# Optimization experiments

Hardware: AMD Instinct MI355X
Metric: run time of the kernel (lower is better)

## Reference

```python
import jax, jax.numpy as jnp
import numpy as np

B, C, D, Hh, W = 2, 320, 4, 16, 16
N = D * Hh * W          # 1024 nodes
NH = 8                  # num_heads
DH = C // NH            # 40
L = 2                   # num_layers
A, EPD = 16, 64         # da_prior tokens, encode_prior_dim
EDGE_SCALE = 32 ** -0.5 # GraphEdgeFeature dim_head=32
SCALE = DH ** -0.5
EPS = 1e-5


def _ln(x, g, b):
    m = x.mean(-1, keepdims=True)
    v = ((x - m) ** 2).mean(-1, keepdims=True)
    return (x - m) * jax.lax.rsqrt(v + EPS) * g + b


def setup_inputs() -> dict:
    key = jax.random.key(0)
    ks = jax.random.split(key, 16)
    std = 0.02 / np.sqrt(L)
    inp = {
        'x': jax.random.normal(ks[0], (B, C, D, Hh, W), jnp.float32),
        'da_prior': jax.random.normal(ks[1], (B, A, EPD), jnp.float32),
        # GraphEdgeFeature.to_qk (no bias), init std 0.02/sqrt(24)
        'qk_w': jax.random.normal(ks[2], (2 * C, C), jnp.float32) * (0.02 / np.sqrt(24)),
        # fc_prior
        'fcp_w': jax.random.normal(ks[3], (C, EPD), jnp.float32) * 0.02,
        'fcp_b': jnp.zeros((C,), jnp.float32),
        # per-layer (stacked over L)
        'ln1_g': jnp.ones((L, C), jnp.float32),
        'ln1_b': jnp.zeros((L, C), jnp.float32),
        'gln_g': jnp.ones((L, C), jnp.float32),
        'gln_b': jnp.zeros((L, C), jnp.float32),
        'qkv_w': jax.random.normal(ks[4], (L, 3 * C, C), jnp.float32) * std,
        'qkv_b': jnp.zeros((L, 3 * C), jnp.float32),
        'proj_w': jax.random.normal(ks[5], (L, C, C), jnp.float32) * std,
        'proj_b': jnp.zeros((L, C), jnp.float32),
        # expand Conv2d(1, NH, 1): weight [NH], bias [NH]
        'exp_w': jax.random.normal(ks[6], (L, NH), jnp.float32),
        'exp_b': jnp.zeros((L, NH), jnp.float32),
        # reduce Conv2d(NH, 1, 1): weight [NH], bias scalar
        'red_w': jax.random.normal(ks[7], (L, NH), jnp.float32) / np.sqrt(NH),
        'red_b': jnp.zeros((L,), jnp.float32),
    }
    return inp


def _forward(x, da_prior, qk_w, fcp_w, fcp_b, ln1_g, ln1_b, gln_g, gln_b,
             qkv_w, qkv_b, proj_w, proj_b, exp_w, exp_b, red_w, red_b):
    node = x.reshape(B, C, N)                       # [B,C,N]
    # ---- GraphEdgeFeature: full-dim QK attention over nodes ----
    xt = node.transpose(0, 2, 1)                    # [B,N,C]
    qk = xt @ qk_w.T                                # [B,N,2C]
    q_e, k_e = jnp.split(qk, 2, axis=-1)
    edge = jax.nn.softmax(jnp.einsum('bqc,bkc->bqk', q_e, k_e) * EDGE_SCALE, axis=-1)  # [B,N,N]
    # ---- fc_prior ----
    da = da_prior @ fcp_w.T + fcp_b                 # [B,A,C]
    s = da.sum(axis=1)                              # [B,C] (sum over 'a' in einsum bnc,bca->bnc)
    for l in range(L):
        # block norm1 over channel dim
        nt = _ln(node.transpose(0, 2, 1), ln1_g[l], ln1_b[l])   # [B,N,C]
        # torch.einsum('bnn,bnc->bnc') takes the DIAGONAL of edge
        diag = jnp.diagonal(edge, axis1=1, axis2=2)             # [B,N]
        node2 = diag[:, :, None] * nt * s[:, None, :] + nt      # [B,N,C]
        y = _ln(node2, gln_g[l], gln_b[l])
        qkv = (y @ qkv_w[l].T + qkv_b[l]).reshape(B, N, 3, NH, DH)
        qkv = qkv.transpose(2, 0, 3, 1, 4)                      # [3,B,H,N,DH]
        q, k, v = qkv[0], qkv[1], qkv[2]
        attn = jnp.einsum('bhnd,bhmd->bhnm', q, k) * SCALE
        attn = attn + edge[:, None] * exp_w[l][None, :, None, None] + exp_b[l][None, :, None, None]
        a = jax.nn.softmax(attn, axis=-1)                       # [B,H,N,N]
        node_out = jnp.einsum('bhnm,bhmd->bhnd', a, v).transpose(0, 2, 1, 3).reshape(B, N, C)
        edge_new = jnp.einsum('bhnm,h->bnm', a + attn, red_w[l]) + red_b[l]  # [B,N,N]
        ws = jax.nn.softmax(edge_new, axis=-1)
        wsum = (ws * edge_new).sum(-1)                          # [B,N]
        node_out = node_out + wsum[:, :, None]                  # fc=Identity, broadcast
        node_out = node_out @ proj_w[l].T + proj_b[l]
        node = node_out.transpose(0, 2, 1)                      # [B,C,N]
        edge = edge + edge_new
    return node.reshape(B, C, D, Hh, W)


def reference(x, da_prior, qk_w, fcp_w, fcp_b, ln1_g, ln1_b, gln_g, gln_b,
              qkv_w, qkv_b, proj_w, proj_b, exp_w, exp_b, red_w, red_b):
    return _forward(x, da_prior, qk_w, fcp_w, fcp_b, ln1_g, ln1_b, gln_g, gln_b,
                    qkv_w, qkv_b, proj_w, proj_b, exp_w, exp_b, red_w, red_b)
```

## Files before the change

### kernel.cpp

```cpp
#include <hip/hip_runtime.h>
#include <math.h>

#define EDGE_SCALE 0.17677669529663687f
#define ATT_SCALE  0.15811388300841897f
#define LN_EPS 1e-5f

typedef __attribute__((ext_vector_type(8))) short bf8;
typedef __attribute__((ext_vector_type(4))) float f32x4;

__device__ __forceinline__ f32x4 mfma16(bf8 a, bf8 b, f32x4 c) {
  return __builtin_amdgcn_mfma_f32_16x16x32_bf16(a, b, c, 0, 0, 0);
}
__device__ __forceinline__ unsigned short f2bf(float f) {
  union { float f; unsigned u; } v; v.f = f;
  unsigned r = v.u + 0x7FFF + ((v.u >> 16) & 1);
  return (unsigned short)(r >> 16);
}
__device__ __forceinline__ float bf2f(unsigned short h) {
  union { unsigned u; float f; } v; v.u = ((unsigned)h) << 16;
  return v.f;
}
__device__ __forceinline__ float wave_max(float v) {
  #pragma unroll
  for (int o = 32; o > 0; o >>= 1) v = fmaxf(v, __shfl_xor(v, o));
  return v;
}
__device__ __forceinline__ float wave_sum(float v) {
  #pragma unroll
  for (int o = 32; o > 0; o >>= 1) v += __shfl_xor(v, o);
  return v;
}

__global__ __launch_bounds__(256) void k_trans(const float* __restrict__ x,
    float* __restrict__ node, unsigned short* __restrict__ nodebf) {
  __shared__ float tile[32][33];
  const int b = blockIdx.z;
  const int n0 = blockIdx.x * 32, c0 = blockIdx.y * 32;
  const int tx = threadIdx.x & 31, ty = threadIdx.x >> 5;
  #pragma unroll
  for (int k = 0; k < 4; ++k) {
    int c = c0 + ty + 8 * k;
    tile[ty + 8 * k][tx] = x[((size_t)b * 320 + c) * 1024 + n0 + tx];
  }
  __syncthreads();
  #pragma unroll
  for (int k = 0; k < 4; ++k) {
    int n = n0 + ty + 8 * k;
    float v = tile[tx][ty + 8 * k];
    size_t idx = ((size_t)b * 1024 + n) * 320 + c0 + tx;
    node[idx] = v;
    nodebf[idx] = f2bf(v);
  }
}

__global__ __launch_bounds__(320) void k_svec(const float* __restrict__ da,
    const float* __restrict__ fw, const float* __restrict__ fb, float* __restrict__ sv) {
  __shared__ float ds[64];
  const int b = blockIdx.x, t = threadIdx.x;
  if (t < 64) {
    float a = 0.f;
    #pragma unroll
    for (int i = 0; i < 16; ++i) a += da[b * 1024 + i * 64 + t];
    ds[t] = a;
  }
  __syncthreads();
  if (t < 320) {
    float acc = 16.f * fb[t];
    #pragma unroll
    for (int e = 0; e < 64; ++e) acc = fmaf(ds[e], fw[t * 64 + e], acc);
    sv[b * 320 + t] = acc;
  }
}

__global__ void k_wcvt(const float* __restrict__ a, int na,
                       const float* __restrict__ b, int nb,
                       const float* __restrict__ c, int nc,
                       unsigned short* __restrict__ out) {
  int tot = na + nb + nc;
  for (int i = blockIdx.x * blockDim.x + threadIdx.x; i < tot; i += gridDim.x * blockDim.x) {
    float v = (i < na) ? a[i] : ((i < na + nb) ? b[i - na] : c[i - na - nb]);
    out[i] = f2bf(v);
  }
}

__global__ __launch_bounds__(256, 4) void k_mgemm(
    const unsigned short* __restrict__ A, const unsigned short* __restrict__ W,
    const float* __restrict__ bias, void* p0, void* p1, void* p2, int mode) {
  __shared__ float smem[64 * 65];
  const int t = threadIdx.x, w = t >> 6, lane = t & 63;
  const int q16 = lane >> 4, l16 = lane & 15;
  const int rt = blockIdx.x * 64, jt = blockIdx.y * 64;
  f32x4 acc[4];
  #pragma unroll
  for (int i = 0; i < 4; ++i)
    #pragma unroll
    for (int j = 0; j < 4; ++j) acc[i][j] = 0.f;
  const unsigned short* ap = A + (size_t)(rt + 16 * w + l16) * 320 + q16 * 8;
  const unsigned short* wp = W + (size_t)(jt + l16) * 320 + q16 * 8;
  for (int kc = 0; kc < 10; ++kc) {
    bf8 af = *(const bf8*)(ap + kc * 32);
    #pragma unroll
    for (int ct = 0; ct < 4; ++ct) {
      bf8 bf = *(const bf8*)(wp + (size_t)ct * 16 * 320 + kc * 32);
      acc[ct] = mfma16(af, bf, acc[ct]);
    }
  }
  if (mode == 0 || mode == 1) {
    #pragma unroll
    for (int ct = 0; ct < 4; ++ct) {
      int col = jt + ct * 16 + l16;
      float bv = bias ? bias[col] : 0.f;
      #pragma unroll
      for (int r = 0; r < 4; ++r) {
        int row = rt + 16 * w + q16 * 4 + r;
        float v = acc[ct][r] + bv;
        if (mode == 0) {
          ((float*)p0)[(size_t)row * 320 + col] = v;
        } else {
          if (col < 320) ((unsigned short*)p0)[(size_t)row * 320 + col] = f2bf(v);
          else           ((unsigned short*)p1)[(size_t)row * 320 + col - 320] = f2bf(v);
        }
      }
    }
  } else if (mode == 2) {
    const int part = jt / 320;
    if (part < 2) {
      unsigned short* dst = (unsigned short*)(part == 0 ? p0 : p1);
      #pragma unroll
      for (int ct = 0; ct < 4; ++ct) {
        int col = jt + ct * 16 + l16;
        float bv = bias[col];
        int rem = col - part * 320;
        int h = rem / 40, d = rem % 40;
        #pragma unroll
        for (int r = 0; r < 4; ++r) {
          int row = rt + 16 * w + q16 * 4 + r;
          int b = row >> 10, n = row & 1023;
          size_t base = (((size_t)b * 8 + h) * 1024 + n) * 64;
          dst[base + d] = f2bf(acc[ct][r] + bv);
          if (d < 24) dst[base + 40 + d] = 0;
        }
      }
    } else {
      unsigned short* vt_t = (unsigned short*)smem;
      #pragma unroll
      for (int ct = 0; ct < 4; ++ct) {
        int col = jt + ct * 16 + l16;
        float bv = bias[col];
        #pragma unroll
        for (int r = 0; r < 4; ++r)
          vt_t[(ct * 16 + l16) * 72 + 16 * w + q16 * 4 + r] = f2bf(acc[ct][r] + bv);
      }
      __syncthreads();
      const int cl = t >> 2, seg = t & 3;
      int rem = (jt - 640) + cl;
      int h = rem / 40, d = rem % 40;
      int b = rt >> 10, n = (rt & 1023) + seg * 16;
      const float4* lp = (const float4*)&vt_t[cl * 72 + seg * 16];
      float4 a0 = lp[0], a1 = lp[1];
      float4* gp = (float4*)((unsigned short*)p2 +
                             (((size_t)b * 8 + h) * 48 + d) * 1024 + n);
      gp[0] = a0; gp[1] = a1;
    }
  } else {
    #pragma unroll
    for (int ct = 0; ct < 4; ++ct) {
      int col = jt + ct * 16 + l16;
      float bv = bias[col];
      #pragma unroll
      for (int r = 0; r < 4; ++r)
        smem[(16 * w + q16 * 4 + r) * 65 + ct * 16 + l16] = acc[ct][r] + bv;
    }
    __syncthreads();
    const int cl = t >> 2, seg = t & 3;
    int b = rt >> 10, n = (rt & 1023) + seg * 16;
    float* orow = (float*)p0 + ((size_t)b * 320 + jt + cl) * 1024 + n;
    #pragma unroll
    for (int i2 = 0; i2 < 4; ++i2) {
      float4 vv;
      vv.x = smem[(seg * 16 + i2 * 4 + 0) * 65 + cl];
      vv.y = smem[(seg * 16 + i2 * 4 + 1) * 65 + cl];
      vv.z = smem[(seg * 16 + i2 * 4 + 2) * 65 + cl];
      vv.w = smem[(seg * 16 + i2 * 4 + 3) * 65 + cl];
      ((float4*)orow)[i2] = vv;
    }
  }
}

__global__ __launch_bounds__(256, 4) void k_sgemm(
    const unsigned short* __restrict__ qe, const unsigned short* __restrict__ ke,
    float* __restrict__ S) {
  const int t = threadIdx.x, w = t >> 6, lane = t & 63;
  const int q16 = lane >> 4, l16 = lane & 15;
  const int rt = blockIdx.x * 64, jt = blockIdx.y * 64, b = blockIdx.z;
  const unsigned short* A = qe + (size_t)b * 1024 * 320;
  const unsigned short* W = ke + (size_t)b * 1024 * 320;
  f32x4 acc[4];
  #pragma unroll
  for (int i = 0; i < 4; ++i)
    #pragma unroll
    for (int j = 0; j < 4; ++j) acc[i][j] = 0.f;
  const unsigned short* ap = A + (size_t)(rt + 16 * w + l16) * 320 + q16 * 8;
  const unsigned short* wp = W + (size_t)(jt + l16) * 320 + q16 * 8;
  for (int kc = 0; kc < 10; ++kc) {
    bf8 af = *(const bf8*)(ap + kc * 32);
    #pragma unroll
    for (int ct = 0; ct < 4; ++ct) {
      bf8 bf = *(const bf8*)(wp + (size_t)ct * 16 * 320 + kc * 32);
      acc[ct] = mfma16(af, bf, acc[ct]);
    }
  }
  #pragma unroll
  for (int ct = 0; ct < 4; ++ct)
    #pragma unroll
    for (int r = 0; r < 4; ++r)
      S[((size_t)b * 1024 + rt + 16 * w + q16 * 4 + r) * 1024 + jt + ct * 16 + l16] =
          acc[ct][r] * EDGE_SCALE;
}

__global__ __launch_bounds__(256) void k_smax(const float* __restrict__ S,
                                              float* __restrict__ edge) {
  const int w = threadIdx.x >> 6, lane = threadIdx.x & 63;
  const int row = blockIdx.x * 4 + w;
  const float4* sp = (const float4*)(S + (size_t)row * 1024) + lane;
  float4 v[4];
  #pragma unroll
  for (int i = 0; i < 4; ++i) v[i] = sp[i * 64];
  float mx = -3.4e38f;
  #pragma unroll
  for (int i = 0; i < 4; ++i)
    mx = fmaxf(mx, fmaxf(fmaxf(v[i].x, v[i].y), fmaxf(v[i].z, v[i].w)));
  mx = wave_max(mx);
  float s = 0.f;
  #pragma unroll
  for (int i = 0; i < 4; ++i) {
    v[i].x = __expf(v[i].x - mx); v[i].y = __expf(v[i].y - mx);
    v[i].z = __expf(v[i].z - mx); v[i].w = __expf(v[i].w - mx);
    s += v[i].x + v[i].y + v[i].z + v[i].w;
  }
  s = wave_sum(s);
  float inv = 1.f / s;
  float4* ep = (float4*)(edge + (size_t)row * 1024) + lane;
  #pragma unroll
  for (int i = 0; i < 4; ++i)
    ep[i * 64] = make_float4(v[i].x * inv, v[i].y * inv, v[i].z * inv, v[i].w * inv);
}

__global__ __launch_bounds__(256) void k_ln(const float* __restrict__ node,
    const float* __restrict__ edge, const float* __restrict__ sv,
    const float* __restrict__ g1, const float* __restrict__ b1,
    const float* __restrict__ g2, const float* __restrict__ b2,
    unsigned short* __restrict__ y) {
  const int w = threadIdx.x >> 6, lane = threadIdx.x & 63;
  const int row = blockIdx.x * 4 + w;
  const int b = row >> 10, n = row & 1023;
  const float* xr = node + (size_t)row * 320;
  float x[5];
  #pragma unroll
  for (int i = 0; i < 5; ++i) x[i] = xr[lane + 64 * i];
  float s = x[0] + x[1] + x[2] + x[3] + x[4];
  float mean = wave_sum(s) * (1.f / 320.f);
  float v = 0.f;
  #pragma unroll
  for (int i = 0; i < 5; ++i) { float d = x[i] - mean; v += d * d; }
  float rstd = rsqrtf(wave_sum(v) * (1.f / 320.f) + LN_EPS);
  float diag = edge[(size_t)row * 1024 + n];
  float n2[5];
  #pragma unroll
  for (int i = 0; i < 5; ++i) {
    int c = lane + 64 * i;
    float nt = (x[i] - mean) * rstd * g1[c] + b1[c];
    n2[i] = diag * nt * sv[b * 320 + c] + nt;
  }
  s = n2[0] + n2[1] + n2[2] + n2[3] + n2[4];
  float mean2 = wave_sum(s) * (1.f / 320.f);
  v = 0.f;
  #pragma unroll
  for (int i = 0; i < 5; ++i) { float d = n2[i] - mean2; v += d * d; }
  float rstd2 = rsqrtf(wave_sum(v) * (1.f / 320.f) + LN_EPS);
  unsigned short* yr = y + (size_t)row * 320;
  #pragma unroll
  for (int i = 0; i < 5; ++i) {
    int c = lane + 64 * i;
    yr[c] = f2bf((n2[i] - mean2) * rstd2 * g2[c] + b2[c]);
  }
}

__global__ __launch_bounds__(256, 4) void k_score(
    const unsigned short* __restrict__ qbf, const unsigned short* __restrict__ kbf,
    const unsigned short* __restrict__ vtb, const float* __restrict__ edge,
    unsigned short* __restrict__ thbuf, float* __restrict__ att,
    const float* __restrict__ ew, const float* __restrict__ eb,
    const float* __restrict__ rw) {
  __shared__ unsigned short a_lds[4][4][16][20];
  __shared__ unsigned short th_lds[4][16][72];
  __shared__ float ored[4][3][16][17];
  __shared__ float redm[4][16], reds[4][16];
  const int t = threadIdx.x, w = t >> 6, lane = t & 63;
  const int q16 = lane >> 4, l16 = lane & 15;
  const int n0 = blockIdx.x * 16, h = blockIdx.y, b = blockIdx.z;
  const size_t bh = (size_t)b * 8 + h;
  const unsigned short* qp = qbf + (bh * 1024 + n0 + l16) * 64 + q16 * 8;
  bf8 af0 = *(const bf8*)(qp);
  bf8 af1 = *(const bf8*)(qp + 32);
  f32x4 acc[16];
  #pragma unroll
  for (int i = 0; i < 16; ++i)
    #pragma unroll
    for (int j = 0; j < 4; ++j) acc[i][j] = 0.f;
  const unsigned short* kp = kbf + (bh * 1024 + (size_t)w * 256 + l16) * 64 + q16 * 8;
  #pragma unroll
  for (int tt = 0; tt < 16; ++tt) {
    const unsigned short* kpt = kp + (size_t)tt * 16 * 64;
    bf8 b0 = *(const bf8*)(kpt);
    bf8 b1 = *(const bf8*)(kpt + 32);
    acc[tt] = mfma16(af0, b0, acc[tt]);
    acc[tt] = mfma16(af1, b1, acc[tt]);
  }
  const float ewh = ew[h], ebh = eb[h], rwh = rw[h];
  const float* ep = edge + ((size_t)b * 1024 + n0 + q16 * 4) * 1024 + w * 256 + l16;
  #pragma unroll
  for (int tt = 0; tt < 16; ++tt)
    #pragma unroll
    for (int r = 0; r < 4; ++r) {
      float ev = ep[(size_t)r * 1024 + tt * 16];
      acc[tt][r] = fmaf(acc[tt][r], ATT_SCALE, fmaf(ev, ewh, ebh));
    }
  float pm[4] = {-3.4e38f, -3.4e38f, -3.4e38f, -3.4e38f};
  #pragma unroll
  for (int tt = 0; tt < 16; ++tt)
    #pragma unroll
    for (int r = 0; r < 4; ++r) pm[r] = fmaxf(pm[r], acc[tt][r]);
  #pragma unroll
  for (int r = 0; r < 4; ++r)
    #pragma unroll
    for (int o = 1; o <= 8; o <<= 1) pm[r] = fmaxf(pm[r], __shfl_xor(pm[r], o));
  if (l16 == 0) {
    #pragma unroll
    for (int r = 0; r < 4; ++r) redm[w][q16 * 4 + r] = pm[r];
  }
  __syncthreads();
  float m[4], ps[4] = {0.f, 0.f, 0.f, 0.f};
  #pragma unroll
  for (int r = 0; r < 4; ++r)
    m[r] = fmaxf(fmaxf(redm[0][q16 * 4 + r], redm[1][q16 * 4 + r]),
                 fmaxf(redm[2][q16 * 4 + r], redm[3][q16 * 4 + r]));
  #pragma unroll
  for (int tt = 0; tt < 16; ++tt)
    #pragma unroll
    for (int r = 0; r < 4; ++r) ps[r] += __expf(acc[tt][r] - m[r]);
  #pragma unroll
  for (int r = 0; r < 4; ++r)
    #pragma unroll
    for (int o = 1; o <= 8; o <<= 1) ps[r] += __shfl_xor(ps[r], o);
  if (l16 == 0) {
    #pragma unroll
    for (int r = 0; r < 4; ++r) reds[w][q16 * 4 + r] = ps[r];
  }
  __syncthreads();
  float inv[4];
  #pragma unroll
  for (int r = 0; r < 4; ++r)
    inv[r] = 1.f / (reds[0][q16 * 4 + r] + reds[1][q16 * 4 + r] +
                    reds[2][q16 * 4 + r] + reds[3][q16 * 4 + r]);
  f32x4 oacc[3];
  #pragma unroll
  for (int i = 0; i < 3; ++i)
    #pragma unroll
    for (int j = 0; j < 4; ++j) oacc[i][j] = 0.f;
  unsigned short* tbase = thbuf + (bh * 1024 + n0) * 1024 + w * 256;
  const int trow = lane >> 2, tc4 = lane & 3;
  #pragma unroll
  for (int g = 0; g < 4; ++g) {
    #pragma unroll
    for (int ti = 0; ti < 4; ++ti) {
      int tt = g * 4 + ti;
      #pragma unroll
      for (int r = 0; r < 4; ++r) {
        float e = __expf(acc[tt][r] - m[r]);
        float a = e * inv[r];
        a_lds[w][ti][q16 * 4 + r][l16] = f2bf(a);
        th_lds[w][q16 * 4 + r][ti * 16 + l16] = f2bf(rwh * (a + acc[tt][r]));
      }
    }
    #pragma unroll
    for (int kk = 0; kk < 2; ++kk) {
      const unsigned short* ap2 = &a_lds[w][kk * 2 + (q16 >> 1)][l16][(q16 & 1) * 8];
      short4 lo = *(const short4*)(ap2);
      short4 hi = *(const short4*)(ap2 + 4);
      bf8 afv = {lo.x, lo.y, lo.z, lo.w, hi.x, hi.y, hi.z, hi.w};
      int kc = w * 8 + g * 2 + kk;
      const unsigned short* vp = vtb + (bh * 48 + l16) * 1024 + (size_t)kc * 32 + q16 * 8;
      #pragma unroll
      for (int nt = 0; nt < 3; ++nt) {
        bf8 bfv = *(const bf8*)(vp + (size_t)nt * 16 * 1024);
        oacc[nt] = mfma16(afv, bfv, oacc[nt]);
      }
    }
    {
      const float4* lp = (const float4*)&th_lds[w][trow][tc4 * 16];
      float4 v0 = lp[0], v1 = lp[1];
      float4* gp = (float4*)(tbase + (size_t)trow * 1024 + g * 64 + tc4 * 16);
      gp[0] = v0; gp[1] = v1;
    }
  }
  #pragma unroll
  for (int nt = 0; nt < 3; ++nt)
    #pragma unroll
    for (int r = 0; r < 4; ++r) ored[w][nt][q16 * 4 + r][l16] = oacc[nt][r];
  __syncthreads();
  #pragma unroll
  for (int k = 0; k < 3; ++k) {
    int o = k * 256 + t;
    int nt = o >> 8, row = (o >> 4) & 15, col = o & 15;
    int dim = nt * 16 + col;
    float sum = ored[0][nt][row][col] + ored[1][nt][row][col] +
                ored[2][nt][row][col] + ored[3][nt][row][col];
    if (dim < 40)
      att[((size_t)b * 1024 + n0 + row) * 320 + h * 40 + dim] = sum;
  }
}

__global__ __launch_bounds__(256) void k_wsum(
    const unsigned short* __restrict__ thbuf, float* __restrict__ edge,
    const float* __restrict__ att, unsigned short* __restrict__ attbf,
    const float* __restrict__ rb) {
  const int w = threadIdx.x >> 6, lane = threadIdx.x & 63;
  const int row = blockIdx.x * 4 + w;
  const int b = row >> 10, n = row & 1023;
  const float rbv = rb[0];
  float tv[16];
  #pragma unroll
  for (int i = 0; i < 16; ++i) tv[i] = rbv;
  #pragma unroll 1
  for (int h = 0; h < 8; ++h) {
    const unsigned short* tph = thbuf + (((size_t)b * 8 + h) * 1024 + n) * 1024 + lane * 4;
    #pragma unroll
    for (int seg = 0; seg < 4; ++seg) {
      ushort4 u = *(const ushort4*)(tph + seg * 256);
      tv[seg * 4 + 0] += bf2f(u.x);
      tv[seg * 4 + 1] += bf2f(u.y);
      tv[seg * 4 + 2] += bf2f(u.z);
      tv[seg * 4 + 3] += bf2f(u.w);
    }
  }
  float4* erp = (float4*)(edge + ((size_t)b * 1024 + n) * 1024) + lane;
  #pragma unroll
  for (int seg = 0; seg < 4; ++seg) {
    float4 e = erp[seg * 64];
    e.x += tv[seg * 4 + 0]; e.y += tv[seg * 4 + 1];
    e.z += tv[seg * 4 + 2]; e.w += tv[seg * 4 + 3];
    erp[seg * 64] = e;
  }
  float mx = -3.4e38f;
  #pragma unroll
  for (int i = 0; i < 16; ++i) mx = fmaxf(mx, tv[i]);
  mx = wave_max(mx);
  float s = 0.f, num = 0.f;
  #pragma unroll
  for (int i = 0; i < 16; ++i) {
    float e = __expf(tv[i] - mx);
    s += e; num += e * tv[i];
  }
  s = wave_sum(s); num = wave_sum(num);
  const float wsum = num / s;
  const float* ar = att + (size_t)row * 320;
  unsigned short* ao = attbf + (size_t)row * 320;
  #pragma unroll
  for (int i = 0; i < 5; ++i) {
    int c = lane + 64 * i;
    ao[c] = f2bf(ar[c] + wsum);
  }
}

extern "C" void kernel_launch(void* const* d_in, const int* in_sizes, int n_in,
                              void* d_out, int out_size, void* d_ws, size_t ws_size,
                              hipStream_t stream) {
  const float* x      = (const float*)d_in[0];
  const float* da     = (const float*)d_in[1];
  const float* qk_w   = (const float*)d_in[2];
  const float* fcp_w  = (const float*)d_in[3];
  const float* fcp_b  = (const float*)d_in[4];
  const float* ln1_g  = (const float*)d_in[5];
  const float* ln1_b  = (const float*)d_in[6];
  const float* gln_g  = (const float*)d_in[7];
  const float* gln_b  = (const float*)d_in[8];
  const float* qkv_w  = (const float*)d_in[9];
  const float* qkv_b  = (const float*)d_in[10];
  const float* proj_w = (const float*)d_in[11];
  const float* proj_b = (const float*)d_in[12];
  const float* exp_w  = (const float*)d_in[13];
  const float* exp_b  = (const float*)d_in[14];
  const float* red_w  = (const float*)d_in[15];
  const float* red_b  = (const float*)d_in[16];
  float* ws = (float*)d_ws;
  float* node  = ws + 0;
  unsigned short* ybf   = (unsigned short*)(ws + 655360);
  float* attb  = ws + 983040;
  unsigned short* attbf = (unsigned short*)(ws + 1638400);
  float* edge  = ws + 1966080;
  float* svec  = ws + 4063232;
  unsigned short* nodebf = (unsigned short*)(ws + 4063872);
  unsigned short* qe   = (unsigned short*)(ws + 4391552);
  unsigned short* ke   = (unsigned short*)(ws + 4719232);
  unsigned short* qbf  = (unsigned short*)(ws + 5046912);
  unsigned short* kbf  = (unsigned short*)(ws + 5571200);
  unsigned short* vtb  = (unsigned short*)(ws + 6095488);
  unsigned short* wbf  = (unsigned short*)(ws + 6488704);
  unsigned short* thbuf= (unsigned short*)(ws + 7000704);
  float* sbuf = ws + 15389312;
  float* out = (float*)d_out;
  unsigned short* qk_wb   = wbf;
  unsigned short* qkv_wb  = wbf + 204800;
  unsigned short* proj_wb = wbf + 819200;

  hipLaunchKernelGGL(k_trans, dim3(32, 10, 2), dim3(256), 0, stream, x, node, nodebf);
  hipLaunchKernelGGL(k_svec, dim3(2), dim3(320), 0, stream, da, fcp_w, fcp_b, svec);
  hipLaunchKernelGGL(k_wcvt, dim3(512), dim3(256), 0, stream,
                     qk_w, 204800, qkv_w, 614400, proj_w, 204800, wbf);
  hipLaunchKernelGGL(k_mgemm, dim3(32, 10), dim3(256), 0, stream,
                     nodebf, qk_wb, (const float*)nullptr, qe, ke, (void*)nullptr, 1);
  hipLaunchKernelGGL(k_sgemm, dim3(16, 16, 2), dim3(256), 0, stream, qe, ke, sbuf);
  hipLaunchKernelGGL(k_smax, dim3(512), dim3(256), 0, stream, sbuf, edge);
  for (int l = 0; l < 2; ++l) {
    hipLaunchKernelGGL(k_ln, dim3(512), dim3(256), 0, stream, node, edge, svec,
                       ln1_g + l * 320, ln1_b + l * 320, gln_g + l * 320, gln_b + l * 320, ybf);
    hipLaunchKernelGGL(k_mgemm, dim3(32, 15), dim3(256), 0, stream,
                       ybf, qkv_wb + (size_t)l * 307200, qkv_b + l * 960, qbf, kbf, vtb, 2);
    hipLaunchKernelGGL(k_score, dim3(64, 8, 2), dim3(256), 0, stream,
                       qbf, kbf, vtb, edge, thbuf, attb,
                       exp_w + l * 8, exp_b + l * 8, red_w + l * 8);
    hipLaunchKernelGGL(k_wsum, dim3(512), dim3(256), 0, stream,
                       thbuf, edge, attb, attbf, red_b + l);
    if (l == 0)
      hipLaunchKernelGGL(k_mgemm, dim3(32, 5), dim3(256), 0, stream,
                         attbf, proj_wb, proj_b, node, (void*)nullptr, (void*)nullptr, 0);
    else
      hipLaunchKernelGGL(k_mgemm, dim3(32, 5), dim3(256), 0, stream,
                         attbf, proj_wb + 102400, proj_b + 320, out,
                         (void*)nullptr, (void*)nullptr, 3);
  }
}
```

Before: 292.4 us.

## Fuse per-head score kernel with edge-update and wsum kernel, looping heads in-block

Merges the attention-score kernel and the edge-sum/softmax kernel into one kernel. Each 512-thread block owns 16 query rows of one batch, loops over all 8 heads, and accumulates the reduced edge update in registers. This removes the large bf16 per-head edge buffer that was written to global memory and read back, and the fp32 attention round trip. The cost is far fewer blocks (128 instead of 1024 plus 512), so the heads are processed serially inside each block and parallelism across CUs drops.

```diff
diff --git a/kernel.cpp b/kernel.cpp
--- a/kernel.cpp
+++ b/kernel.cpp
@@ -286,190 +286,230 @@
   }
 }
 
-__global__ __launch_bounds__(256, 4) void k_score(
+__global__ __launch_bounds__(512, 2) void k_fused(
     const unsigned short* __restrict__ qbf, const unsigned short* __restrict__ kbf,
-    const unsigned short* __restrict__ vtb, const float* __restrict__ edge,
-    unsigned short* __restrict__ thbuf, float* __restrict__ att,
+    const unsigned short* __restrict__ vtb, float* __restrict__ edge,
+    unsigned short* __restrict__ attbf,
     const float* __restrict__ ew, const float* __restrict__ eb,
-    const float* __restrict__ rw) {
-  __shared__ unsigned short a_lds[4][4][16][20];
-  __shared__ unsigned short th_lds[4][16][72];
-  __shared__ float ored[4][3][16][17];
-  __shared__ float redm[4][16], reds[4][16];
+    const float* __restrict__ rw, const float* __restrict__ rb) {
+  __shared__ unsigned short a_lds[8][8][16][20];
+  __shared__ float ored[8][3][16][17];
+  __shared__ float att_lds[16][328];
+  __shared__ float redm[8][16], reds[8][16], redn[8][16];
+  __shared__ float wsum_lds[16];
   const int t = threadIdx.x, w = t >> 6, lane = t & 63;
   const int q16 = lane >> 4, l16 = lane & 15;
-  const int n0 = blockIdx.x * 16, h = blockIdx.y, b = blockIdx.z;
-  const size_t bh = (size_t)b * 8 + h;
-  const unsigned short* qp = qbf + (bh * 1024 + n0 + l16) * 64 + q16 * 8;
-  bf8 af0 = *(const bf8*)(qp);
-  bf8 af1 = *(const bf8*)(qp + 32);
-  f32x4 acc[16];
-  #pragma unroll
-  for (int i = 0; i < 16; ++i)
-    #pragma unroll
-    for (int j = 0; j < 4; ++j) acc[i][j] = 0.f;
-  const unsigned short* kp = kbf + (bh * 1024 + (size_t)w * 256 + l16) * 64 + q16 * 8;
-  #pragma unroll
-  for (int tt = 0; tt < 16; ++tt) {
-    const unsigned short* kpt = kp + (size_t)tt * 16 * 64;
-    bf8 b0 = *(const bf8*)(kpt);
-    bf8 b1 = *(const bf8*)(kpt + 32);
-    acc[tt] = mfma16(af0, b0, acc[tt]);
-    acc[tt] = mfma16(af1, b1, acc[tt]);
-  }
-  const float ewh = ew[h], ebh = eb[h], rwh = rw[h];
-  const float* ep = edge + ((size_t)b * 1024 + n0 + q16 * 4) * 1024 + w * 256 + l16;
-  #pragma unroll
-  for (int tt = 0; tt < 16; ++tt)
+  const int bid = blockIdx.x;
+  const int b = (bid & 7) >> 2;
+  const int tile = ((bid >> 3) << 2) | (bid & 3);
+  const int n0 = tile * 16;
+  const float rbv = rb[0];
+
+  float ev[8][4];
+  const float* ep = edge + ((size_t)b * 1024 + n0 + q16 * 4) * 1024 + w * 128 + l16;
+  #pragma unroll
+  for (int tt = 0; tt < 8; ++tt)
+    #pragma unroll
+    for (int r = 0; r < 4; ++r) ev[tt][r] = ep[(size_t)r * 1024 + tt * 16];
+
+  float tacc[8][4];
+  #pragma unroll
+  for (int tt = 0; tt < 8; ++tt)
+    #pragma unroll
+    for (int r = 0; r < 4; ++r) tacc[tt][r] = rbv;
+
+  for (int h = 0; h < 8; ++h) {
+    const size_t bh = (size_t)b * 8 + h;
+    const unsigned short* qp = qbf + (bh * 1024 + n0 + l16) * 64 + q16 * 8;
+    bf8 af0 = *(const bf8*)(qp);
+    bf8 af1 = *(const bf8*)(qp + 32);
+    f32x4 acc[8];
+    #pragma unroll
+    for (int i = 0; i < 8; ++i)
+      #pragma unroll
+      for (int j = 0; j < 4; ++j) acc[i][j] = 0.f;
+    const unsigned short* kp = kbf + (bh * 1024 + (size_t)w * 128 + l16) * 64 + q16 * 8;
+    #pragma unroll
+    for (int tt = 0; tt < 8; ++tt) {
+      const unsigned short* kpt = kp + (size_t)tt * 16 * 64;
+      bf8 b0 = *(const bf8*)(kpt);
+      bf8 b1 = *(const bf8*)(kpt + 32);
+      acc[tt] = mfma16(af0, b0, acc[tt]);
+      acc[tt] = mfma16(af1, b1, acc[tt]);
+    }
+    const float ewh = ew[h], ebh = eb[h], rwh = rw[h];
+    #pragma unroll
+    for (int tt = 0; tt < 8; ++tt)
+      #pragma unroll
+      for (int r = 0; r < 4; ++r)
+        acc[tt][r] = fmaf(acc[tt][r], ATT_SCALE, fmaf(ev[tt][r], ewh, ebh));
+    float pm[4] = {-3.4e38f, -3.4e38f, -3.4e38f, -3.4e38f};
+    #pragma unroll
+    for (int tt = 0; tt < 8; ++tt)
+      #pragma unroll
+      for (int r = 0; r < 4; ++r) pm[r] = fmaxf(pm[r], acc[tt][r]);
+    #pragma unroll
+    for (int r = 0; r < 4; ++r)
+      #pragma unroll
+      for (int o = 1; o <= 8; o <<= 1) pm[r] = fmaxf(pm[r], __shfl_xor(pm[r], o));
+    if (l16 == 0) {
+      #pragma unroll
+      for (int r = 0; r < 4; ++r) redm[w][q16 * 4 + r] = pm[r];
+    }
+    __syncthreads();
+    float m4[4], ps[4] = {0.f, 0.f, 0.f, 0.f};
     #pragma unroll
     for (int r = 0; r < 4; ++r) {
-      float ev = ep[(size_t)r * 1024 + tt * 16];
-      acc[tt][r] = fmaf(acc[tt][r], ATT_SCALE, fmaf(ev, ewh, ebh));
-    }
-  float pm[4] = {-3.4e38f, -3.4e38f, -3.4e38f, -3.4e38f};
-  #pragma unroll
-  for (int tt = 0; tt < 16; ++tt)
-    #pragma unroll
-    for (int r = 0; r < 4; ++r) pm[r] = fmaxf(pm[r], acc[tt][r]);
-  #pragma unroll
-  for (int r = 0; r < 4; ++r)
-    #pragma unroll
-    for (int o = 1; o <= 8; o <<= 1) pm[r] = fmaxf(pm[r], __shfl_xor(pm[r], o));
-  if (l16 == 0) {
-    #pragma unroll
-    for (int r = 0; r < 4; ++r) redm[w][q16 * 4 + r] = pm[r];
-  }
-  __syncthreads();
-  float m[4], ps[4] = {0.f, 0.f, 0.f, 0.f};
-  #pragma unroll
-  for (int r = 0; r < 4; ++r)
-    m[r] = fmaxf(fmaxf(redm[0][q16 * 4 + r], redm[1][q16 * 4 + r]),
-                 fmaxf(redm[2][q16 * 4 + r], redm[3][q16 * 4 + r]));
-  #pragma unroll
-  for (int tt = 0; tt < 16; ++tt)
-    #pragma unroll
-    for (int r = 0; r < 4; ++r) ps[r] += __expf(acc[tt][r] - m[r]);
-  #pragma unroll
-  for (int r = 0; r < 4; ++r)
-    #pragma unroll
-    for (int o = 1; o <= 8; o <<= 1) ps[r] += __shfl_xor(ps[r], o);
-  if (l16 == 0) {
-    #pragma unroll
-    for (int r = 0; r < 4; ++r) reds[w][q16 * 4 + r] = ps[r];
-  }
-  __syncthreads();
-  float inv[4];
-  #pragma unroll
-  for (int r = 0; r < 4; ++r)
-    inv[r] = 1.f / (reds[0][q16 * 4 + r] + reds[1][q16 * 4 + r] +
-                    reds[2][q16 * 4 + r] + reds[3][q16 * 4 + r]);
-  f32x4 oacc[3];
-  #pragma unroll
-  for (int i = 0; i < 3; ++i)
-    #pragma unroll
-    for (int j = 0; j < 4; ++j) oacc[i][j] = 0.f;
-  unsigned short* tbase = thbuf + (bh * 1024 + n0) * 1024 + w * 256;
-  const int trow = lane >> 2, tc4 = lane & 3;
-  #pragma unroll
-  for (int g = 0; g < 4; ++g) {
-    #pragma unroll
-    for (int ti = 0; ti < 4; ++ti) {
-      int tt = g * 4 + ti;
+      float mm = redm[0][q16 * 4 + r];
+      #pragma unroll
+      for (int wv = 1; wv < 8; ++wv) mm = fmaxf(mm, redm[wv][q16 * 4 + r]);
+      m4[r] = mm;
+    }
+    #pragma unroll
+    for (int tt = 0; tt < 8; ++tt)
+      #pragma unroll
+      for (int r = 0; r < 4; ++r) ps[r] += __expf(acc[tt][r] - m4[r]);
+    #pragma unroll
+    for (int r = 0; r < 4; ++r)
+      #pragma unroll
+      for (int o = 1; o <= 8; o <<= 1) ps[r] += __shfl_xor(ps[r], o);
+    if (l16 == 0) {
+      #pragma unroll
+      for (int r = 0; r < 4; ++r) reds[w][q16 * 4 + r] = ps[r];
+    }
+    __syncthreads();
+    float inv[4];
+    #pragma unroll
+    for (int r = 0; r < 4; ++r) {
+      float ss = reds[0][q16 * 4 + r];
+      #pragma unroll
+      for (int wv = 1; wv < 8; ++wv) ss += reds[wv][q16 * 4 + r];
+      inv[r] = 1.f / ss;
+    }
+    #pragma unroll
+    for (int tt = 0; tt < 8; ++tt)
       #pragma unroll
       for (int r = 0; r < 4; ++r) {
-        float e = __expf(acc[tt][r] - m[r]);
+        float e = __expf(acc[tt][r] - m4[r]);
         float a = e * inv[r];
-        a_lds[w][ti][q16 * 4 + r][l16] = f2bf(a);
-        th_lds[w][q16 * 4 + r][ti * 16 + l16] = f2bf(rwh * (a + acc[tt][r]));
-      }
-    }
-    #pragma unroll
-    for (int kk = 0; kk < 2; ++kk) {
+        tacc[tt][r] += rwh * (a + acc[tt][r]);
+        a_lds[w][tt][q16 * 4 + r][l16] = f2bf(a);
+      }
+    f32x4 oacc[3];
+    #pragma unroll
+    for (int i = 0; i < 3; ++i)
+      #pragma unroll
+      for (int j = 0; j < 4; ++j) oacc[i][j] = 0.f;
+    #pragma unroll
+    for (int kk = 0; kk < 4; ++kk) {
       const unsigned short* ap2 = &a_lds[w][kk * 2 + (q16 >> 1)][l16][(q16 & 1) * 8];
       short4 lo = *(const short4*)(ap2);
       short4 hi = *(const short4*)(ap2 + 4);
       bf8 afv = {lo.x, lo.y, lo.z, lo.w, hi.x, hi.y, hi.z, hi.w};
-      int kc = w * 8 + g * 2 + kk;
-      const unsigned short* vp = vtb + (bh * 48 + l16) * 1024 + (size_t)kc * 32 + q16 * 8;
+      const unsigned short* vp = vtb + (bh * 48 + l16) * 1024 + (size_t)w * 128 + kk * 32 + q16 * 8;
       #pragma unroll
       for (int nt = 0; nt < 3; ++nt) {
         bf8 bfv = *(const bf8*)(vp + (size_t)nt * 16 * 1024);
         oacc[nt] = mfma16(afv, bfv, oacc[nt]);
       }
     }
+    #pragma unroll
+    for (int nt = 0; nt < 3; ++nt)
+      #pragma unroll
+      for (int r = 0; r < 4; ++r) ored[w][nt][q16 * 4 + r][l16] = oacc[nt][r];
+    __syncthreads();
     {
-      const float4* lp = (const float4*)&th_lds[w][trow][tc4 * 16];
-      float4 v0 = lp[0], v1 = lp[1];
-      float4* gp = (float4*)(tbase + (size_t)trow * 1024 + g * 64 + tc4 * 16);
-      gp[0] = v0; gp[1] = v1;
-    }
-  }
-  #pragma unroll
-  for (int nt = 0; nt < 3; ++nt)
-    #pragma unroll
-    for (int r = 0; r < 4; ++r) ored[w][nt][q16 * 4 + r][l16] = oacc[nt][r];
-  __syncthreads();
-  #pragma unroll
-  for (int k = 0; k < 3; ++k) {
-    int o = k * 256 + t;
-    int nt = o >> 8, row = (o >> 4) & 15, col = o & 15;
-    int dim = nt * 16 + col;
-    float sum = ored[0][nt][row][col] + ored[1][nt][row][col] +
-                ored[2][nt][row][col] + ored[3][nt][row][col];
-    if (dim < 40)
-      att[((size_t)b * 1024 + n0 + row) * 320 + h * 40 + dim] = sum;
-  }
-}
-
-__global__ __launch_bounds__(256) void k_wsum(
-    const unsigned short* __restrict__ thbuf, float* __restrict__ edge,
-    const float* __restrict__ att, unsigned short* __restrict__ attbf,
-    const float* __restrict__ rb) {
-  const int w = threadIdx.x >> 6, lane = threadIdx.x & 63;
-  const int row = blockIdx.x * 4 + w;
-  const int b = row >> 10, n = row & 1023;
-  const float rbv = rb[0];
-  float tv[16];
-  #pragma unroll
-  for (int i = 0; i < 16; ++i) tv[i] = rbv;
-  #pragma unroll 1
-  for (int h = 0; h < 8; ++h) {
-    const unsigned short* tph = thbuf + (((size_t)b * 8 + h) * 1024 + n) * 1024 + lane * 4;
-    #pragma unroll
-    for (int seg = 0; seg < 4; ++seg) {
-      ushort4 u = *(const ushort4*)(tph + seg * 256);
-      tv[seg * 4 + 0] += bf2f(u.x);
-      tv[seg * 4 + 1] += bf2f(u.y);
-      tv[seg * 4 + 2] += bf2f(u.z);
-      tv[seg * 4 + 3] += bf2f(u.w);
-    }
-  }
-  float4* erp = (float4*)(edge + ((size_t)b * 1024 + n) * 1024) + lane;
-  #pragma unroll
-  for (int seg = 0; seg < 4; ++seg) {
-    float4 e = erp[seg * 64];
-    e.x += tv[seg * 4 + 0]; e.y += tv[seg * 4 + 1];
-    e.z += tv[seg * 4 + 2]; e.w += tv[seg * 4 + 3];
-    erp[seg * 64] = e;
-  }
-  float mx = -3.4e38f;
-  #pragma unroll
-  for (int i = 0; i < 16; ++i) mx = fmaxf(mx, tv[i]);
-  mx = wave_max(mx);
-  float s = 0.f, num = 0.f;
-  #pragma unroll
-  for (int i = 0; i < 16; ++i) {
-    float e = __expf(tv[i] - mx);
-    s += e; num += e * tv[i];
-  }
-  s = wave_sum(s); num = wave_sum(num);
-  const float wsum = num / s;
-  const float* ar = att + (size_t)row * 320;
-  unsigned short* ao = attbf + (size_t)row * 320;
-  #pragma unroll
-  for (int i = 0; i < 5; ++i) {
-    int c = lane + 64 * i;
-    ao[c] = f2bf(ar[c] + wsum);
+      int idx = t;
+      int nt = idx >> 8, row = (idx >> 4) & 15, col = idx & 15;
+      int dim = nt * 16 + col;
+      float sum = 0.f;
+      #pragma unroll
+      for (int wv = 0; wv < 8; ++wv) sum += ored[wv][nt][row][col];
+      if (dim < 40) att_lds[row][h * 40 + dim] = sum;
+    }
+    if (t < 256) {
+      int idx = 512 + t;
+      int nt = idx >> 8, row = (idx >> 4) & 15, col = idx & 15;
+      int dim = nt * 16 + col;
+      float sum = 0.f;
+      #pragma unroll
+      for (int wv = 0; wv < 8; ++wv) sum += ored[wv][nt][row][col];
+      if (dim < 40) att_lds[row][h * 40 + dim] = sum;
+    }
+  }
+
+  {
+    float pm[4] = {-3.4e38f, -3.4e38f, -3.4e38f, -3.4e38f};
+    #pragma unroll
+    for (int tt = 0; tt < 8; ++tt)
+      #pragma unroll
+      for (int r = 0; r < 4; ++r) pm[r] = fmaxf(pm[r], tacc[tt][r]);
+    #pragma unroll
+    for (int r = 0; r < 4; ++r)
+      #pragma unroll
+      for (int o = 1; o <= 8; o <<= 1) pm[r] = fmaxf(pm[r], __shfl_xor(pm[r], o));
+    if (l16 == 0) {
+      #pragma unroll
+      for (int r = 0; r < 4; ++r) redm[w][q16 * 4 + r] = pm[r];
+    }
+    __syncthreads();
+    float m4[4], s4[4] = {0.f, 0.f, 0.f, 0.f}, n4[4] = {0.f, 0.f, 0.f, 0.f};
+    #pragma unroll
+    for (int r = 0; r < 4; ++r) {
+      float mm = redm[0][q16 * 4 + r];
+      #pragma unroll
+      for (int wv = 1; wv < 8; ++wv) mm = fmaxf(mm, redm[wv][q16 * 4 + r]);
+      m4[r] = mm;
+    }
+    #pragma unroll
+    for (int tt = 0; tt < 8; ++tt)
+      #pragma unroll
+      for (int r = 0; r < 4; ++r) {
+        float e = __expf(tacc[tt][r] - m4[r]);
+        s4[r] += e;
+        n4[r] += e * tacc[tt][r];
+      }
+    #pragma unroll
+    for (int r = 0; r < 4; ++r)
+      #pragma unroll
+      for (int o = 1; o <= 8; o <<= 1) {
+        s4[r] += __shfl_xor(s4[r], o);
+        n4[r] += __shfl_xor(n4[r], o);
+      }
+    if (l16 == 0) {
+      #pragma unroll
+      for (int r = 0; r < 4; ++r) {
+        reds[w][q16 * 4 + r] = s4[r];
+        redn[w][q16 * 4 + r] = n4[r];
+      }
+    }
+    __syncthreads();
+    float* epo = edge + ((size_t)b * 1024 + n0 + q16 * 4) * 1024 + w * 128 + l16;
+    #pragma unroll
+    for (int tt = 0; tt < 8; ++tt)
+      #pragma unroll
+      for (int r = 0; r < 4; ++r)
+        epo[(size_t)r * 1024 + tt * 16] = ev[tt][r] + tacc[tt][r];
+    if (w == 0 && l16 == 0) {
+      #pragma unroll
+      for (int r = 0; r < 4; ++r) {
+        float ss = 0.f, nn = 0.f;
+        #pragma unroll
+        for (int wv = 0; wv < 8; ++wv) {
+          ss += reds[wv][q16 * 4 + r];
+          nn += redn[wv][q16 * 4 + r];
+        }
+        wsum_lds[q16 * 4 + r] = nn / ss;
+      }
+    }
+    __syncthreads();
+    unsigned short* ab = attbf + ((size_t)b * 1024 + n0) * 320;
+    #pragma unroll
+    for (int i = 0; i < 10; ++i) {
+      int idx = i * 512 + t;
+      int row = idx / 320, c = idx - row * 320;
+      ab[(size_t)row * 320 + c] = f2bf(att_lds[row][c] + wsum_lds[row]);
+    }
   }
 }
 
@@ -496,7 +536,6 @@
   float* ws = (float*)d_ws;
   float* node  = ws + 0;
   unsigned short* ybf   = (unsigned short*)(ws + 655360);
-  float* attb  = ws + 983040;
   unsigned short* attbf = (unsigned short*)(ws + 1638400);
   float* edge  = ws + 1966080;
   float* svec  = ws + 4063232;
@@ -507,7 +546,6 @@
   unsigned short* kbf  = (unsigned short*)(ws + 5571200);
   unsigned short* vtb  = (unsigned short*)(ws + 6095488);
   unsigned short* wbf  = (unsigned short*)(ws + 6488704);
-  unsigned short* thbuf= (unsigned short*)(ws + 7000704);
   float* sbuf = ws + 15389312;
   float* out = (float*)d_out;
   unsigned short* qk_wb   = wbf;
@@ -527,11 +565,9 @@
                        ln1_g + l * 320, ln1_b + l * 320, gln_g + l * 320, gln_b + l * 320, ybf);
     hipLaunchKernelGGL(k_mgemm, dim3(32, 15), dim3(256), 0, stream,
                        ybf, qkv_wb + (size_t)l * 307200, qkv_b + l * 960, qbf, kbf, vtb, 2);
-    hipLaunchKernelGGL(k_score, dim3(64, 8, 2), dim3(256), 0, stream,
-                       qbf, kbf, vtb, edge, thbuf, attb,
-                       exp_w + l * 8, exp_b + l * 8, red_w + l * 8);
-    hipLaunchKernelGGL(k_wsum, dim3(512), dim3(256), 0, stream,
-                       thbuf, edge, attb, attbf, red_b + l);
+    hipLaunchKernelGGL(k_fused, dim3(128), dim3(512), 0, stream,
+                       qbf, kbf, vtb, edge, attbf,
+                       exp_w + l * 8, exp_b + l * 8, red_w + l * 8, red_b + l);
     if (l == 0)
       hipLaunchKernelGGL(k_mgemm, dim3(32, 5), dim3(256), 0, stream,
                          attbf, proj_wb, proj_b, node, (void*)nullptr, (void*)nullptr, 0);
```

Measured after the change: 341.3 us. +16.7%, slower.

## Process head pairs per block to halve edge-term intermediate traffic

Applied to the files above, without the earlier changes.

Each score block now handles two heads for the same query tile and accumulates the reduce-weighted edge contribution in registers, writing one partial per head pair instead of one per head. This halves the bf16 intermediate written by the score kernel and read by the wsum kernel. The block index is also remapped so blocks sharing a tile and batch land on the same XCD, which should improve L2 reuse of the edge rows. In exchange, occupancy drops (launch bounds 4 to 2) because of the extra 64-float accumulator, and each block now runs the two heads one after the other.

```diff
diff --git a/kernel.cpp b/kernel.cpp
--- a/kernel.cpp
+++ b/kernel.cpp
@@ -286,10 +286,10 @@
   }
 }
 
-__global__ __launch_bounds__(256, 4) void k_score(
+__global__ __launch_bounds__(256, 2) void k_score2(
     const unsigned short* __restrict__ qbf, const unsigned short* __restrict__ kbf,
     const unsigned short* __restrict__ vtb, const float* __restrict__ edge,
-    unsigned short* __restrict__ thbuf, float* __restrict__ att,
+    unsigned short* __restrict__ thb, float* __restrict__ att,
     const float* __restrict__ ew, const float* __restrict__ eb,
     const float* __restrict__ rw) {
   __shared__ unsigned short a_lds[4][4][16][20];
@@ -298,77 +298,135 @@
   __shared__ float redm[4][16], reds[4][16];
   const int t = threadIdx.x, w = t >> 6, lane = t & 63;
   const int q16 = lane >> 4, l16 = lane & 15;
-  const int n0 = blockIdx.x * 16, h = blockIdx.y, b = blockIdx.z;
-  const size_t bh = (size_t)b * 8 + h;
-  const unsigned short* qp = qbf + (bh * 1024 + n0 + l16) * 64 + q16 * 8;
-  bf8 af0 = *(const bf8*)(qp);
-  bf8 af1 = *(const bf8*)(qp + 32);
-  f32x4 acc[16];
+  const int bid = blockIdx.x;
+  const int xcd = bid & 7, idx = bid >> 3;
+  const int b = idx >> 5;
+  const int tile = xcd * 8 + ((idx >> 2) & 7);
+  const int hp = idx & 3;
+  const int n0 = tile * 16;
+  float tacc[16][4];
   #pragma unroll
   for (int i = 0; i < 16; ++i)
     #pragma unroll
-    for (int j = 0; j < 4; ++j) acc[i][j] = 0.f;
-  const unsigned short* kp = kbf + (bh * 1024 + (size_t)w * 256 + l16) * 64 + q16 * 8;
-  #pragma unroll
-  for (int tt = 0; tt < 16; ++tt) {
-    const unsigned short* kpt = kp + (size_t)tt * 16 * 64;
-    bf8 b0 = *(const bf8*)(kpt);
-    bf8 b1 = *(const bf8*)(kpt + 32);
-    acc[tt] = mfma16(af0, b0, acc[tt]);
-    acc[tt] = mfma16(af1, b1, acc[tt]);
-  }
-  const float ewh = ew[h], ebh = eb[h], rwh = rw[h];
-  const float* ep = edge + ((size_t)b * 1024 + n0 + q16 * 4) * 1024 + w * 256 + l16;
-  #pragma unroll
-  for (int tt = 0; tt < 16; ++tt)
-    #pragma unroll
-    for (int r = 0; r < 4; ++r) {
-      float ev = ep[(size_t)r * 1024 + tt * 16];
-      acc[tt][r] = fmaf(acc[tt][r], ATT_SCALE, fmaf(ev, ewh, ebh));
-    }
-  float pm[4] = {-3.4e38f, -3.4e38f, -3.4e38f, -3.4e38f};
-  #pragma unroll
-  for (int tt = 0; tt < 16; ++tt)
-    #pragma unroll
-    for (int r = 0; r < 4; ++r) pm[r] = fmaxf(pm[r], acc[tt][r]);
-  #pragma unroll
-  for (int r = 0; r < 4; ++r)
-    #pragma unroll
-    for (int o = 1; o <= 8; o <<= 1) pm[r] = fmaxf(pm[r], __shfl_xor(pm[r], o));
-  if (l16 == 0) {
-    #pragma unroll
-    for (int r = 0; r < 4; ++r) redm[w][q16 * 4 + r] = pm[r];
-  }
-  __syncthreads();
-  float m[4], ps[4] = {0.f, 0.f, 0.f, 0.f};
-  #pragma unroll
-  for (int r = 0; r < 4; ++r)
-    m[r] = fmaxf(fmaxf(redm[0][q16 * 4 + r], redm[1][q16 * 4 + r]),
-                 fmaxf(redm[2][q16 * 4 + r], redm[3][q16 * 4 + r]));
-  #pragma unroll
-  for (int tt = 0; tt < 16; ++tt)
-    #pragma unroll
-    for (int r = 0; r < 4; ++r) ps[r] += __expf(acc[tt][r] - m[r]);
-  #pragma unroll
-  for (int r = 0; r < 4; ++r)
-    #pragma unroll
-    for (int o = 1; o <= 8; o <<= 1) ps[r] += __shfl_xor(ps[r], o);
-  if (l16 == 0) {
-    #pragma unroll
-    for (int r = 0; r < 4; ++r) reds[w][q16 * 4 + r] = ps[r];
-  }
-  __syncthreads();
-  float inv[4];
-  #pragma unroll
-  for (int r = 0; r < 4; ++r)
-    inv[r] = 1.f / (reds[0][q16 * 4 + r] + reds[1][q16 * 4 + r] +
-                    reds[2][q16 * 4 + r] + reds[3][q16 * 4 + r]);
-  f32x4 oacc[3];
-  #pragma unroll
-  for (int i = 0; i < 3; ++i)
-    #pragma unroll
-    for (int j = 0; j < 4; ++j) oacc[i][j] = 0.f;
-  unsigned short* tbase = thbuf + (bh * 1024 + n0) * 1024 + w * 256;
+    for (int r = 0; r < 4; ++r) tacc[i][r] = 0.f;
+
+  for (int h2 = 0; h2 < 2; ++h2) {
+    const int h = hp * 2 + h2;
+    const size_t bh = (size_t)b * 8 + h;
+    const unsigned short* qp = qbf + (bh * 1024 + n0 + l16) * 64 + q16 * 8;
+    bf8 af0 = *(const bf8*)(qp);
+    bf8 af1 = *(const bf8*)(qp + 32);
+    f32x4 acc[16];
+    #pragma unroll
+    for (int i = 0; i < 16; ++i)
+      #pragma unroll
+      for (int j = 0; j < 4; ++j) acc[i][j] = 0.f;
+    const unsigned short* kp = kbf + (bh * 1024 + (size_t)w * 256 + l16) * 64 + q16 * 8;
+    #pragma unroll
+    for (int tt = 0; tt < 16; ++tt) {
+      const unsigned short* kpt = kp + (size_t)tt * 16 * 64;
+      bf8 b0 = *(const bf8*)(kpt);
+      bf8 b1 = *(const bf8*)(kpt + 32);
+      acc[tt] = mfma16(af0, b0, acc[tt]);
+      acc[tt] = mfma16(af1, b1, acc[tt]);
+    }
+    const float ewh = ew[h], ebh = eb[h], rwh = rw[h];
+    const float* ep = edge + ((size_t)b * 1024 + n0 + q16 * 4) * 1024 + w * 256 + l16;
+    #pragma unroll
+    for (int tt = 0; tt < 16; ++tt)
+      #pragma unroll
+      for (int r = 0; r < 4; ++r) {
+        float ev = ep[(size_t)r * 1024 + tt * 16];
+        acc[tt][r] = fmaf(acc[tt][r], ATT_SCALE, fmaf(ev, ewh, ebh));
+      }
+    float pm[4] = {-3.4e38f, -3.4e38f, -3.4e38f, -3.4e38f};
+    #pragma unroll
+    for (int tt = 0; tt < 16; ++tt)
+      #pragma unroll
+      for (int r = 0; r < 4; ++r) pm[r] = fmaxf(pm[r], acc[tt][r]);
+    #pragma unroll
+    for (int r = 0; r < 4; ++r)
+      #pragma unroll
+      for (int o = 1; o <= 8; o <<= 1) pm[r] = fmaxf(pm[r], __shfl_xor(pm[r], o));
+    if (l16 == 0) {
+      #pragma unroll
+      for (int r = 0; r < 4; ++r) redm[w][q16 * 4 + r] = pm[r];
+    }
+    __syncthreads();
+    float m[4], ps[4] = {0.f, 0.f, 0.f, 0.f};
+    #pragma unroll
+    for (int r = 0; r < 4; ++r)
+      m[r] = fmaxf(fmaxf(redm[0][q16 * 4 + r], redm[1][q16 * 4 + r]),
+                   fmaxf(redm[2][q16 * 4 + r], redm[3][q16 * 4 + r]));
+    #pragma unroll
+    for (int tt = 0; tt < 16; ++tt)
+      #pragma unroll
+      for (int r = 0; r < 4; ++r) ps[r] += __expf(acc[tt][r] - m[r]);
+    #pragma unroll
+    for (int r = 0; r < 4; ++r)
+      #pragma unroll
+      for (int o = 1; o <= 8; o <<= 1) ps[r] += __shfl_xor(ps[r], o);
+    if (l16 == 0) {
+      #pragma unroll
+      for (int r = 0; r < 4; ++r) reds[w][q16 * 4 + r] = ps[r];
+    }
+    __syncthreads();
+    float inv[4];
+    #pragma unroll
+    for (int r = 0; r < 4; ++r)
+      inv[r] = 1.f / (reds[0][q16 * 4 + r] + reds[1][q16 * 4 + r] +
+                      reds[2][q16 * 4 + r] + reds[3][q16 * 4 + r]);
+    f32x4 oacc[3];
+    #pragma unroll
+    for (int i = 0; i < 3; ++i)
+      #pragma unroll
+      for (int j = 0; j < 4; ++j) oacc[i][j] = 0.f;
+    #pragma unroll
+    for (int g = 0; g < 4; ++g) {
+      #pragma unroll
+      for (int ti = 0; ti < 4; ++ti) {
+        int tt = g * 4 + ti;
+        #pragma unroll
+        for (int r = 0; r < 4; ++r) {
+          float e = __expf(acc[tt][r] - m[r]);
+          float a = e * inv[r];
+          tacc[tt][r] += rwh * (a + acc[tt][r]);
+          a_lds[w][ti][q16 * 4 + r][l16] = f2bf(a);
+        }
+      }
+      #pragma unroll
+      for (int kk = 0; kk < 2; ++kk) {
+        const unsigned short* ap2 = &a_lds[w][kk * 2 + (q16 >> 1)][l16][(q16 & 1) * 8];
+        short4 lo = *(const short4*)(ap2);
+        short4 hi = *(const short4*)(ap2 + 4);
+        bf8 afv = {lo.x, lo.y, lo.z, lo.w, hi.x, hi.y, hi.z, hi.w};
+        int kc = w * 8 + g * 2 + kk;
+        const unsigned short* vp = vtb + (bh * 48 + l16) * 1024 + (size_t)kc * 32 + q16 * 8;
+        #pragma unroll
+        for (int nt = 0; nt < 3; ++nt) {
+          bf8 bfv = *(const bf8*)(vp + (size_t)nt * 16 * 1024);
+          oacc[nt] = mfma16(afv, bfv, oacc[nt]);
+        }
+      }
+    }
+    #pragma unroll
+    for (int nt = 0; nt < 3; ++nt)
+      #pragma unroll
+      for (int r = 0; r < 4; ++r) ored[w][nt][q16 * 4 + r][l16] = oacc[nt][r];
+    __syncthreads();
+    #pragma unroll
+    for (int k = 0; k < 3; ++k) {
+      int o = k * 256 + t;
+      int nt = o >> 8, row = (o >> 4) & 15, col = o & 15;
+      int dim = nt * 16 + col;
+      float sum = ored[0][nt][row][col] + ored[1][nt][row][col] +
+                  ored[2][nt][row][col] + ored[3][nt][row][col];
+      if (dim < 40)
+        att[((size_t)b * 1024 + n0 + row) * 320 + h * 40 + dim] = sum;
+    }
+  }
+
+  unsigned short* tbase = thb + (((size_t)b * 4 + hp) * 1024 + n0) * 1024 + w * 256;
   const int trow = lane >> 2, tc4 = lane & 3;
   #pragma unroll
   for (int g = 0; g < 4; ++g) {
@@ -376,53 +434,18 @@
     for (int ti = 0; ti < 4; ++ti) {
       int tt = g * 4 + ti;
       #pragma unroll
-      for (int r = 0; r < 4; ++r) {
-        float e = __expf(acc[tt][r] - m[r]);
-        float a = e * inv[r];
-        a_lds[w][ti][q16 * 4 + r][l16] = f2bf(a);
-        th_lds[w][q16 * 4 + r][ti * 16 + l16] = f2bf(rwh * (a + acc[tt][r]));
-      }
-    }
-    #pragma unroll
-    for (int kk = 0; kk < 2; ++kk) {
-      const unsigned short* ap2 = &a_lds[w][kk * 2 + (q16 >> 1)][l16][(q16 & 1) * 8];
-      short4 lo = *(const short4*)(ap2);
-      short4 hi = *(const short4*)(ap2 + 4);
-      bf8 afv = {lo.x, lo.y, lo.z, lo.w, hi.x, hi.y, hi.z, hi.w};
-      int kc = w * 8 + g * 2 + kk;
-      const unsigned short* vp = vtb + (bh * 48 + l16) * 1024 + (size_t)kc * 32 + q16 * 8;
-      #pragma unroll
-      for (int nt = 0; nt < 3; ++nt) {
-        bf8 bfv = *(const bf8*)(vp + (size_t)nt * 16 * 1024);
-        oacc[nt] = mfma16(afv, bfv, oacc[nt]);
-      }
-    }
-    {
-      const float4* lp = (const float4*)&th_lds[w][trow][tc4 * 16];
-      float4 v0 = lp[0], v1 = lp[1];
-      float4* gp = (float4*)(tbase + (size_t)trow * 1024 + g * 64 + tc4 * 16);
-      gp[0] = v0; gp[1] = v1;
-    }
-  }
-  #pragma unroll
-  for (int nt = 0; nt < 3; ++nt)
-    #pragma unroll
-    for (int r = 0; r < 4; ++r) ored[w][nt][q16 * 4 + r][l16] = oacc[nt][r];
-  __syncthreads();
-  #pragma unroll
-  for (int k = 0; k < 3; ++k) {
-    int o = k * 256 + t;
-    int nt = o >> 8, row = (o >> 4) & 15, col = o & 15;
-    int dim = nt * 16 + col;
-    float sum = ored[0][nt][row][col] + ored[1][nt][row][col] +
-                ored[2][nt][row][col] + ored[3][nt][row][col];
-    if (dim < 40)
-      att[((size_t)b * 1024 + n0 + row) * 320 + h * 40 + dim] = sum;
-  }
-}
-
-__global__ __launch_bounds__(256) void k_wsum(
-    const unsigned short* __restrict__ thbuf, float* __restrict__ edge,
+      for (int r = 0; r < 4; ++r)
+        th_lds[w][q16 * 4 + r][ti * 16 + l16] = f2bf(tacc[tt][r]);
+    }
+    const float4* lp = (const float4*)&th_lds[w][trow][tc4 * 16];
+    float4 v0 = lp[0], v1 = lp[1];
+    float4* gp = (float4*)(tbase + (size_t)trow * 1024 + g * 64 + tc4 * 16);
+    gp[0] = v0; gp[1] = v1;
+  }
+}
+
+__global__ __launch_bounds__(256) void k_wsum2(
+    const unsigned short* __restrict__ thb, float* __restrict__ edge,
     const float* __restrict__ att, unsigned short* __restrict__ attbf,
     const float* __restrict__ rb) {
   const int w = threadIdx.x >> 6, lane = threadIdx.x & 63;
@@ -433,8 +456,8 @@
   #pragma unroll
   for (int i = 0; i < 16; ++i) tv[i] = rbv;
   #pragma unroll 1
-  for (int h = 0; h < 8; ++h) {
-    const unsigned short* tph = thbuf + (((size_t)b * 8 + h) * 1024 + n) * 1024 + lane * 4;
+  for (int p = 0; p < 4; ++p) {
+    const unsigned short* tph = thb + (((size_t)b * 4 + p) * 1024 + n) * 1024 + lane * 4;
     #pragma unroll
     for (int seg = 0; seg < 4; ++seg) {
       ushort4 u = *(const ushort4*)(tph + seg * 256);
@@ -527,10 +550,10 @@
                        ln1_g + l * 320, ln1_b + l * 320, gln_g + l * 320, gln_b + l * 320, ybf);
     hipLaunchKernelGGL(k_mgemm, dim3(32, 15), dim3(256), 0, stream,
                        ybf, qkv_wb + (size_t)l * 307200, qkv_b + l * 960, qbf, kbf, vtb, 2);
-    hipLaunchKernelGGL(k_score, dim3(64, 8, 2), dim3(256), 0, stream,
+    hipLaunchKernelGGL(k_score2, dim3(512), dim3(256), 0, stream,
                        qbf, kbf, vtb, edge, thbuf, attb,
                        exp_w + l * 8, exp_b + l * 8, red_w + l * 8);
-    hipLaunchKernelGGL(k_wsum, dim3(512), dim3(256), 0, stream,
+    hipLaunchKernelGGL(k_wsum2, dim3(512), dim3(256), 0, stream,
                        thbuf, edge, attb, attbf, red_b + l);
     if (l == 0)
       hipLaunchKernelGGL(k_mgemm, dim3(32, 5), dim3(256), 0, stream,
```

Result: slower. 339.2 us (+16.0%).
